# Performance work log

Hardware: AMD Instinct MI355X
Metric: run time of the kernel (lower is better)

The kernel has to match this reference:

```python
import jax, jax.numpy as jnp
import numpy as np

BS, S, DM, H = 4, 512, 512, 8
DK = DM // H
EPS = 1e-6


def setup_inputs() -> dict:
    key = jax.random.key(0)
    ks = jax.random.split(key, 11)
    sc = jnp.float32(0.02)  # small init so exp(q @ k^T) stays finite (no max-subtraction in original)
    return {
        "q": jax.random.normal(ks[0], (BS, S, DM), jnp.float32),
        "k": jax.random.normal(ks[1], (BS, S, DM), jnp.float32),
        "v": jax.random.normal(ks[2], (BS, S, DM), jnp.float32),
        "Wq": sc * jax.random.normal(ks[3], (DM, DM), jnp.float32),
        "bq": jnp.zeros((DM,), jnp.float32),
        "Wk": sc * jax.random.normal(ks[4], (DM, DM), jnp.float32),
        "bk": jnp.zeros((DM,), jnp.float32),
        "Wv": sc * jax.random.normal(ks[5], (DM, DM), jnp.float32),
        "bv": jnp.zeros((DM,), jnp.float32),
        "Wo": sc * jax.random.normal(ks[6], (DM, DM), jnp.float32),
        "bo": jnp.zeros((DM,), jnp.float32),
        "alpha": jnp.ones((DK,), jnp.float32),   # Norm.alpha over last dim (= d_k per head)
        "beta": jnp.zeros((DK,), jnp.float32),   # Norm.bias
    }


def reference(q, k, v, Wq, bq, Wk, bk, Wv, bv, Wo, bo, alpha, beta):
    # project and split heads: [bs, h, s, d_k]
    qh = (q @ Wq + bq).reshape(BS, S, H, DK).transpose(0, 2, 1, 3)
    kh = (k @ Wk + bk).reshape(BS, S, H, DK).transpose(0, 2, 1, 3)
    vh = (v @ Wv + bv).reshape(BS, S, H, DK).transpose(0, 2, 1, 3)

    # pairwise-batch exp scores: E[bq, bk, h, i, j] = exp(q[bq] @ k[bk]^T)
    E = jnp.exp(jnp.einsum('bhid,chjd->bchij', qh, kh))  # [BS, BS, H, S, S]
    # fenmu: sum over k-batch, each term scaled by sqrt(d_k) (as in original loop)
    fenmu = jnp.sqrt(jnp.float32(DK)) * E.sum(axis=1)     # [BS, H, S, S]
    # fenzi: same-batch exp scores (diagonal of pairwise tensor)
    fenzi = E[jnp.arange(BS), jnp.arange(BS)]             # [BS, H, S, S]
    R = fenzi / fenmu                                     # [BS, H, S, S]

    # per v-batch-entry score: score[bq, c] = R[bq] @ v[c]
    score = jnp.einsum('bhij,chjd->bchid', R, vh)         # [BS, BS, H, S, DK]
    sm = jax.nn.softmax(score, axis=-1)
    # Norm: torch.std is unbiased (ddof=1); eps added to std, not variance
    mu = sm.mean(axis=-1, keepdims=True)
    std = jnp.sqrt(sm.var(axis=-1, ddof=1, keepdims=True))
    ln = alpha * (sm - mu) / (std + EPS) + beta

    # output += LN(score) + q, accumulated over the v-batch loop (BS iterations)
    heads = ln.sum(axis=1) + jnp.float32(BS) * qh         # [BS, H, S, DK]
    concat = heads.transpose(0, 2, 1, 3).reshape(BS, S, DM)
    return concat @ Wo + bo
```

## Files before the change

### kernel.cpp

```cpp
#include <hip/hip_runtime.h>
#include <hip/hip_bf16.h>

#define BSZ 4
#define SEQ 512
#define DMODEL 512
#define NHEAD 8
#define DKH 64
#define EPSLN 1e-6f

typedef short bf16x8 __attribute__((ext_vector_type(8)));
typedef float f32x4 __attribute__((ext_vector_type(4)));

static __device__ __forceinline__ short f2bf(float x) {
  unsigned u = __builtin_bit_cast(unsigned, x);
  u = (u + 0x7FFFu + ((u >> 16) & 1u)) >> 16;
  return (short)u;
}
static __device__ __forceinline__ bf16x8 cvt8(float4 a, float4 b) {
  bf16x8 r;
  r[0] = f2bf(a.x); r[1] = f2bf(a.y); r[2] = f2bf(a.z); r[3] = f2bf(a.w);
  r[4] = f2bf(b.x); r[5] = f2bf(b.y); r[6] = f2bf(b.z); r[7] = f2bf(b.w);
  return r;
}
static __device__ __forceinline__ unsigned pk2(float a, float b) {
  return (unsigned)(unsigned short)f2bf(a) |
         ((unsigned)(unsigned short)f2bf(b) << 16);
}
static __device__ __forceinline__ void async_cp16(const void* g, void* l) {
  __builtin_amdgcn_global_load_lds(
      (const __attribute__((address_space(1))) unsigned int*)g,
      (__attribute__((address_space(3))) unsigned int*)l, 16, 0, 0);
}

__global__ __launch_bounds__(256) void prep_kernel(
    const float* __restrict__ q, const float* __restrict__ k,
    const float* __restrict__ v, short* __restrict__ qb,
    short* __restrict__ kb, short* __restrict__ vb,
    const float* __restrict__ Wq, const float* __restrict__ Wk,
    const float* __restrict__ Wv, const float* __restrict__ Wo,
    short* __restrict__ Wqt, short* __restrict__ Wkt,
    short* __restrict__ Wvt, short* __restrict__ Wot) {
  __shared__ float T[64][65];
  const int bx = blockIdx.x;
  if (bx < 1536) {
    const int which = bx >> 9, blk = bx & 511;
    const float* s; short* d;
    switch (which) {
      case 0: s = q; d = qb; break;
      case 1: s = k; d = kb; break;
      default: s = v; d = vb; break;
    }
    const size_t idx = (size_t)blk * 2048 + (size_t)threadIdx.x * 8;
    float4 a = *(const float4*)&s[idx];
    float4 b = *(const float4*)&s[idx + 4];
    *(bf16x8*)&d[idx] = cvt8(a, b);
    return;
  }
  const int r = bx - 1536;
  const int mat = r >> 6, m = r & 63;
  const int k0 = (m & 7) * 64, n0 = (m >> 3) * 64;
  const float* src; short* dst;
  switch (mat) {
    case 0: src = Wq; dst = Wqt; break;
    case 1: src = Wk; dst = Wkt; break;
    case 2: src = Wv; dst = Wvt; break;
    default: src = Wo; dst = Wot; break;
  }
  const int tid = threadIdx.x;
  const int n4 = (tid & 15) * 4, kk = tid >> 4;
#pragma unroll
  for (int p = 0; p < 4; ++p) {
    float4 w4 = *(const float4*)&src[(size_t)(k0 + kk + p * 16) * DMODEL + n0 + n4];
    T[kk + p * 16][n4 + 0] = w4.x;
    T[kk + p * 16][n4 + 1] = w4.y;
    T[kk + p * 16][n4 + 2] = w4.z;
    T[kk + p * 16][n4 + 3] = w4.w;
  }
  __syncthreads();
  const int k4 = (tid & 15) * 4;
#pragma unroll
  for (int p = 0; p < 4; ++p) {
    const int nn = (tid >> 4) + p * 16;
    float x0 = T[k4 + 0][nn], x1 = T[k4 + 1][nn];
    float x2 = T[k4 + 2][nn], x3 = T[k4 + 3][nn];
    uint2 u; u.x = pk2(x0, x1); u.y = pk2(x2, x3);
    *(uint2*)&dst[(size_t)(n0 + nn) * DMODEL + k0 + k4] = u;
  }
}

__device__ __forceinline__ void gemm_body(
    const short* __restrict__ A, const short* __restrict__ Wt,
    const float* __restrict__ bias, void* __restrict__ out, int omode) {
  __shared__ short As[2][128 * 32];
  __shared__ short Bs[2][128 * 32];
  const int tid = threadIdx.x;
  const int w = tid >> 6, lane = tid & 63;
  const int l15 = lane & 15, q = lane >> 4;
  const int wm = w >> 1, wn = w & 1;
  const int bn = blockIdx.x * 128, bm = blockIdx.y * 128;
  const int wu = __builtin_amdgcn_readfirstlane(w);
  const int srow = wu * 16 + (lane >> 2);
  const int sch = (lane & 3) ^ ((srow >> 1) & 3);

  f32x4 acc[4][4] = {};

#define GSTAGE(k0, buf)                                                      \
  {                                                                          \
    const short* ga0 = A + (size_t)(bm + srow) * 512 + (k0) + sch * 8;       \
    const short* ga1 = A + (size_t)(bm + srow + 64) * 512 + (k0) + sch * 8;  \
    const short* gb0 = Wt + (size_t)(bn + srow) * 512 + (k0) + sch * 8;      \
    const short* gb1 = Wt + (size_t)(bn + srow + 64) * 512 + (k0) + sch * 8; \
    async_cp16(ga0, &As[buf][wu * 512]);                                     \
    async_cp16(ga1, &As[buf][(4 + wu) * 512]);                               \
    async_cp16(gb0, &Bs[buf][wu * 512]);                                     \
    async_cp16(gb1, &Bs[buf][(4 + wu) * 512]);                               \
  }

  GSTAGE(0, 0);
  for (int ks = 0; ks < 16; ++ks) {
    __syncthreads();
    if (ks < 15) GSTAGE((ks + 1) * 32, (ks + 1) & 1);
    const short* a = As[ks & 1];
    const short* bsh = Bs[ks & 1];
    bf16x8 af[4], bfr[4];
#pragma unroll
    for (int mt = 0; mt < 4; ++mt) {
      const int ra = wm * 64 + mt * 16 + l15;
      af[mt] = *(const bf16x8*)&a[ra * 32 + (q ^ ((ra >> 1) & 3)) * 8];
    }
#pragma unroll
    for (int nt = 0; nt < 4; ++nt) {
      const int rb = wn * 64 + nt * 16 + l15;
      bfr[nt] = *(const bf16x8*)&bsh[rb * 32 + (q ^ ((rb >> 1) & 3)) * 8];
    }
#pragma unroll
    for (int mt = 0; mt < 4; ++mt)
#pragma unroll
      for (int nt = 0; nt < 4; ++nt)
        acc[mt][nt] = __builtin_amdgcn_mfma_f32_16x16x32_bf16(
            af[mt], bfr[nt], acc[mt][nt], 0, 0, 0);
  }
#undef GSTAGE

  float bv[4];
#pragma unroll
  for (int nt = 0; nt < 4; ++nt) bv[nt] = bias[bn + wn * 64 + nt * 16 + l15];
#pragma unroll
  for (int mt = 0; mt < 4; ++mt)
#pragma unroll
    for (int nt = 0; nt < 4; ++nt) {
      const int col = bn + wn * 64 + nt * 16 + l15;
#pragma unroll
      for (int r = 0; r < 4; ++r) {
        const int row = bm + wm * 64 + mt * 16 + q * 4 + r;
        const float val = acc[mt][nt][r] + bv[nt];
        if (omode == 0) {
          ((float*)out)[(size_t)row * 512 + col] = val;
        } else if (omode == 1) {
          ((short*)out)[(size_t)row * 512 + col] = f2bf(val);
        } else {
          const int cc = row >> 9, j = row & 511;
          const int hh = col >> 6, d = col & 63;
          ((short*)out)[(((size_t)(cc * 8 + hh) * 64 + d) << 9) + j] = f2bf(val);
        }
      }
    }
}

__global__ __launch_bounds__(256, 3) void proj_gemm(
    const short* qb, const short* kb, const short* vb,
    const short* Wqt, const short* Wkt, const short* Wvt,
    const float* bq, const float* bk, const float* bvs,
    float* Qp, short* Kb, short* Vt) {
  const short* A; const short* Wt; const float* bias; void* out; int omode;
  switch (blockIdx.z) {
    case 0: A = qb; Wt = Wqt; bias = bq; out = Qp; omode = 0; break;
    case 1: A = kb; Wt = Wkt; bias = bk; out = Kb; omode = 1; break;
    default: A = vb; Wt = Wvt; bias = bvs; out = Vt; omode = 2; break;
  }
  gemm_body(A, Wt, bias, out, omode);
}

__global__ __launch_bounds__(256, 3) void out_gemm(
    const short* Hc, const short* Wot, const float* bo, float* out) {
  gemm_body(Hc, Wot, bo, out, 0);
}

__global__ __launch_bounds__(256, 3) void attn2_kernel(
    const float* __restrict__ Qp, const short* __restrict__ Kb,
    const short* __restrict__ Vt, const float* __restrict__ alpha,
    const float* __restrict__ beta, short* __restrict__ Hc) {
  __shared__ __align__(16) short Stage[2][2 * 4096];
  __shared__ __align__(16) short Rs[32][72];
  __shared__ __align__(16) float xch[16 * 128];

  const int bx = blockIdx.x;
  const int h = bx & 7;
  const int b = (bx >> 3) & 3;
  const int it = bx >> 5;
  const int i0 = it * 32;
  const int tid = threadIdx.x;
  const int w = tid >> 6, lane = tid & 63;
  const int l15 = lane & 15, q = lane >> 4;
  const int wi = w >> 1, wj = w & 1;
  const int wu = __builtin_amdgcn_readfirstlane(w);

  const float* qrow =
      Qp + (size_t)(b * SEQ + i0 + wi * 16 + l15) * DMODEL + h * DKH;
  const bf16x8 aq0 = cvt8(*(const float4*)(qrow + q * 8),
                          *(const float4*)(qrow + q * 8 + 4));
  const bf16x8 aq1 = cvt8(*(const float4*)(qrow + 32 + q * 8),
                          *(const float4*)(qrow + 32 + q * 8 + 4));

  const int srow0 = wu * 8 + (lane >> 3);
  const int scol = (lane & 7) ^ (lane >> 3);

  const short* kbase_h = Kb + h * DKH;
  const short* vbase_h = Vt + (((size_t)h * DKH) << 9);

#define STG1(g0, rs, buf, tslot)                                          \
  {                                                                       \
    async_cp16((g0) + (size_t)srow0 * (rs) + scol * 8,                    \
               &Stage[buf][(tslot) * 4096 + wu * 512]);                   \
    async_cp16((g0) + (size_t)(srow0 + 32) * (rs) + scol * 8,             \
               &Stage[buf][(tslot) * 4096 + (4 + wu) * 512]);             \
  }
#define KTILE(c, j0) (kbase_h + ((size_t)((c) * SEQ) + (j0)) * DMODEL)
#define VTILE(c, j0) (vbase_h + (((size_t)((c) * NHEAD * DKH)) << 9) + (j0))

  f32x4 acc[4][4] = {};
  float sacc[2][4], ebb[2][4];

  STG1(KTILE(0, 0), DMODEL, 0, 0);
  STG1(KTILE(1, 0), DMODEL, 0, 1);

  for (int jt = 0; jt < 8; ++jt) {
    const int j0 = jt * 64;
    bf16x8 ar;
#pragma unroll
    for (int ph2 = 0; ph2 < 4; ++ph2) {
      __syncthreads();
      const int buf = ph2 & 1, nbuf = buf ^ 1;
      if (ph2 == 0) {
        STG1(KTILE(2, j0), DMODEL, nbuf, 0);
        STG1(KTILE(3, j0), DMODEL, nbuf, 1);
      } else if (ph2 == 1) {
        STG1(VTILE(0, j0), SEQ, nbuf, 0);
        STG1(VTILE(1, j0), SEQ, nbuf, 1);
      } else if (ph2 == 2) {
        STG1(VTILE(2, j0), SEQ, nbuf, 0);
        STG1(VTILE(3, j0), SEQ, nbuf, 1);
      } else if (jt < 7) {
        STG1(KTILE(0, j0 + 64), DMODEL, nbuf, 0);
        STG1(KTILE(1, j0 + 64), DMODEL, nbuf, 1);
      }
      if (ph2 < 2) {
        if (ph2 == 0) {
#pragma unroll
          for (int t = 0; t < 2; ++t)
#pragma unroll
            for (int r = 0; r < 4; ++r) { sacc[t][r] = 0.0f; ebb[t][r] = 0.0f; }
        }
#pragma unroll
        for (int ct = 0; ct < 2; ++ct) {
          const int c = ph2 * 2 + ct;
          const short* S = &Stage[buf][ct * 4096];
#pragma unroll
          for (int ntl = 0; ntl < 2; ++ntl) {
            const int row = (wj * 2 + ntl) * 16 + l15;
            const int p0 = q ^ (l15 & 7);
            bf16x8 b0 = *(const bf16x8*)&S[row * 64 + p0 * 8];
            bf16x8 b1 = *(const bf16x8*)&S[row * 64 + (p0 ^ 4) * 8];
            f32x4 s = {};
            s = __builtin_amdgcn_mfma_f32_16x16x32_bf16(aq0, b0, s, 0, 0, 0);
            s = __builtin_amdgcn_mfma_f32_16x16x32_bf16(aq1, b1, s, 0, 0, 0);
#pragma unroll
            for (int r = 0; r < 4; ++r) {
              const float e = __expf(s[r]);
              sacc[ntl][r] += e;
              ebb[ntl][r] = (c == b) ? e : ebb[ntl][r];
            }
          }
        }
        if (ph2 == 1) {
#pragma unroll
          for (int ntl = 0; ntl < 2; ++ntl)
#pragma unroll
            for (int r = 0; r < 4; ++r)
              Rs[wi * 16 + q * 4 + r][(wj * 2 + ntl) * 16 + l15] =
                  f2bf(ebb[ntl][r] / (8.0f * sacc[ntl][r]));
        }
      } else {
        if (ph2 == 2) ar = *(const bf16x8*)&Rs[wi * 16 + l15][wj * 32 + q * 8];
#pragma unroll
        for (int ct = 0; ct < 2; ++ct) {
          const int c = (ph2 - 2) * 2 + ct;
          const short* S = &Stage[buf][ct * 4096];
#pragma unroll
          for (int nt = 0; nt < 4; ++nt) {
            const int row = nt * 16 + l15;
            const int pb = (wj * 4 + q) ^ (l15 & 7);
            bf16x8 bv = *(const bf16x8*)&S[row * 64 + pb * 8];
            acc[c][nt] = __builtin_amdgcn_mfma_f32_16x16x32_bf16(
                ar, bv, acc[c][nt], 0, 0, 0);
          }
        }
      }
    }
  }
#undef STG1
#undef KTILE
#undef VTILE

#pragma unroll
  for (int c = 0; c < BSZ; ++c) {
    if (wj == 1) {
#pragma unroll
      for (int nt = 0; nt < 4; ++nt)
#pragma unroll
        for (int r = 0; r < 4; ++r)
          xch[(nt * 4 + r) * 128 + wi * 64 + lane] = acc[c][nt][r];
    }
    __syncthreads();
    if (wj == 0) {
#pragma unroll
      for (int nt = 0; nt < 4; ++nt)
#pragma unroll
        for (int r = 0; r < 4; ++r)
          acc[c][nt][r] += xch[(nt * 4 + r) * 128 + wi * 64 + lane];
    }
    __syncthreads();
  }

  if (wj == 0) {
    float al[4], be[4];
#pragma unroll
    for (int nt = 0; nt < 4; ++nt) {
      al[nt] = alpha[nt * 16 + l15];
      be[nt] = beta[nt * 16 + l15];
    }
    float hacc[4][4] = {};
#pragma unroll
    for (int c = 0; c < BSZ; ++c) {
#pragma unroll
      for (int r = 0; r < 4; ++r) {
        float e0 = __expf(acc[c][0][r]), e1 = __expf(acc[c][1][r]);
        float e2 = __expf(acc[c][2][r]), e3 = __expf(acc[c][3][r]);
        float es = e0 + e1 + e2 + e3;
#pragma unroll
        for (int m = 8; m >= 1; m >>= 1) es += __shfl_xor(es, m);
        const float inv = 1.0f / es;
        const float d0 = e0 * inv - 0.015625f, d1 = e1 * inv - 0.015625f;
        const float d2 = e2 * inv - 0.015625f, d3 = e3 * inv - 0.015625f;
        float sq = d0 * d0 + d1 * d1 + d2 * d2 + d3 * d3;
#pragma unroll
        for (int m = 8; m >= 1; m >>= 1) sq += __shfl_xor(sq, m);
        const float rs = 1.0f / (sqrtf(sq * (1.0f / 63.0f)) + EPSLN);
        hacc[r][0] += al[0] * d0 * rs + be[0];
        hacc[r][1] += al[1] * d1 * rs + be[1];
        hacc[r][2] += al[2] * d2 * rs + be[2];
        hacc[r][3] += al[3] * d3 * rs + be[3];
      }
    }
#pragma unroll
    for (int r = 0; r < 4; ++r) {
      const size_t rowoff =
          (size_t)(b * SEQ + i0 + wi * 16 + q * 4 + r) * DMODEL + h * DKH;
#pragma unroll
      for (int nt = 0; nt < 4; ++nt) {
        const int d = nt * 16 + l15;
        const float o = hacc[r][nt] + 4.0f * Qp[rowoff + d];
        Hc[rowoff + d] = f2bf(o);
      }
    }
  }
}

extern "C" void kernel_launch(void* const* d_in, const int* in_sizes, int n_in,
                              void* d_out, int out_size, void* d_ws,
                              size_t ws_size, hipStream_t stream) {
  (void)in_sizes; (void)n_in; (void)out_size; (void)ws_size;
  const float* q = (const float*)d_in[0];
  const float* k = (const float*)d_in[1];
  const float* v = (const float*)d_in[2];
  const float* Wq = (const float*)d_in[3];
  const float* bq = (const float*)d_in[4];
  const float* Wk = (const float*)d_in[5];
  const float* bk = (const float*)d_in[6];
  const float* Wv = (const float*)d_in[7];
  const float* bv = (const float*)d_in[8];
  const float* Wo = (const float*)d_in[9];
  const float* bo = (const float*)d_in[10];
  const float* alpha = (const float*)d_in[11];
  const float* beta = (const float*)d_in[12];
  float* out = (float*)d_out;

  char* wsb = (char*)d_ws;
  short* qb = (short*)(wsb);
  short* kb = (short*)(wsb + (2u << 20));
  short* vb = (short*)(wsb + (4u << 20));
  float* Qp = (float*)(wsb + (6u << 20));
  short* Kb = (short*)(wsb + (10u << 20));
  short* Vtg = (short*)(wsb + (12u << 20));
  short* Hc = (short*)(wsb + (14u << 20));
  short* Wqt = (short*)(wsb + (16u << 20));
  short* Wkt = (short*)(wsb + (16u << 20) + (512u << 10));
  short* Wvt = (short*)(wsb + (17u << 20));
  short* Wot = (short*)(wsb + (17u << 20) + (512u << 10));

  prep_kernel<<<dim3(1792), 256, 0, stream>>>(q, k, v, qb, kb, vb,
                                              Wq, Wk, Wv, Wo,
                                              Wqt, Wkt, Wvt, Wot);
  proj_gemm<<<dim3(4, 16, 3), 256, 0, stream>>>(qb, kb, vb, Wqt, Wkt, Wvt,
                                                bq, bk, bv, Qp, Kb, Vtg);
  attn2_kernel<<<dim3(512), 256, 0, stream>>>(Qp, Kb, Vtg, alpha, beta, Hc);
  out_gemm<<<dim3(4, 16), 256, 0, stream>>>(Hc, Wot, bo, out);
}
```

Baseline: 147.1 us.

## Split attention key range across warps with per-warp async ring buffers

Restructures the attention kernel so each of the four warps owns a 32-column slice of the key range for all 32 query rows. Each warp streams its own K/V tiles through a private double-buffered LDS ring, using vmcnt waits in place of block-wide barriers in the main loop. Partial P·V accumulators are then reduced across warps through LDS in a rotated pattern, and each warp computes softmax/LayerNorm for one v-batch. The output is written with vectorized bf16 stores. This trades more registers (launch bounds drop to 2 blocks per SM) and an extra LDS reduction for removing per-phase __syncthreads and reusing each K/V fragment across two query tiles.

```diff
diff --git a/kernel.cpp b/kernel.cpp
--- a/kernel.cpp
+++ b/kernel.cpp
@@ -186,13 +186,12 @@
   gemm_body(Hc, Wot, bo, out, 0);
 }
 
-__global__ __launch_bounds__(256, 3) void attn2_kernel(
+__global__ __launch_bounds__(256, 2) void attn4_kernel(
     const float* __restrict__ Qp, const short* __restrict__ Kb,
     const short* __restrict__ Vt, const float* __restrict__ alpha,
     const float* __restrict__ beta, short* __restrict__ Hc) {
-  __shared__ __align__(16) short Stage[2][2 * 4096];
-  __shared__ __align__(16) short Rs[32][72];
-  __shared__ __align__(16) float xch[16 * 128];
+  __shared__ __align__(16) short Ring[4][2][2048];
+  __shared__ __align__(16) short Rsw[4][32 * 40];
 
   const int bx = blockIdx.x;
   const int h = bx & 7;
@@ -202,150 +201,211 @@
   const int tid = threadIdx.x;
   const int w = tid >> 6, lane = tid & 63;
   const int l15 = lane & 15, q = lane >> 4;
-  const int wi = w >> 1, wj = w & 1;
   const int wu = __builtin_amdgcn_readfirstlane(w);
-
-  const float* qrow =
-      Qp + (size_t)(b * SEQ + i0 + wi * 16 + l15) * DMODEL + h * DKH;
-  const bf16x8 aq0 = cvt8(*(const float4*)(qrow + q * 8),
-                          *(const float4*)(qrow + q * 8 + 4));
-  const bf16x8 aq1 = cvt8(*(const float4*)(qrow + 32 + q * 8),
-                          *(const float4*)(qrow + 32 + q * 8 + 4));
-
-  const int srow0 = wu * 8 + (lane >> 3);
+  short* ring0 = &Ring[wu][0][0];
+  short* ring1 = &Ring[wu][1][0];
+  short* rsw = &Rsw[wu][0];
+
+  bf16x8 aq[2][2];
+#pragma unroll
+  for (int mi = 0; mi < 2; ++mi) {
+    const float* qrow =
+        Qp + (size_t)(b * SEQ + i0 + mi * 16 + l15) * DMODEL + h * DKH;
+    aq[mi][0] = cvt8(*(const float4*)(qrow + q * 8),
+                     *(const float4*)(qrow + q * 8 + 4));
+    aq[mi][1] = cvt8(*(const float4*)(qrow + 32 + q * 8),
+                     *(const float4*)(qrow + 32 + q * 8 + 4));
+  }
+
   const int scol = (lane & 7) ^ (lane >> 3);
-
-  const short* kbase_h = Kb + h * DKH;
-  const short* vbase_h = Vt + (((size_t)h * DKH) << 9);
-
-#define STG1(g0, rs, buf, tslot)                                          \
-  {                                                                       \
-    async_cp16((g0) + (size_t)srow0 * (rs) + scol * 8,                    \
-               &Stage[buf][(tslot) * 4096 + wu * 512]);                   \
-    async_cp16((g0) + (size_t)(srow0 + 32) * (rs) + scol * 8,             \
-               &Stage[buf][(tslot) * 4096 + (4 + wu) * 512]);             \
-  }
-#define KTILE(c, j0) (kbase_h + ((size_t)((c) * SEQ) + (j0)) * DMODEL)
-#define VTILE(c, j0) (vbase_h + (((size_t)((c) * NHEAD * DKH)) << 9) + (j0))
-
-  f32x4 acc[4][4] = {};
-  float sacc[2][4], ebb[2][4];
-
-  STG1(KTILE(0, 0), DMODEL, 0, 0);
-  STG1(KTILE(1, 0), DMODEL, 0, 1);
-
-  for (int jt = 0; jt < 8; ++jt) {
-    const int j0 = jt * 64;
-    bf16x8 ar;
-#pragma unroll
-    for (int ph2 = 0; ph2 < 4; ++ph2) {
-      __syncthreads();
-      const int buf = ph2 & 1, nbuf = buf ^ 1;
-      if (ph2 == 0) {
-        STG1(KTILE(2, j0), DMODEL, nbuf, 0);
-        STG1(KTILE(3, j0), DMODEL, nbuf, 1);
-      } else if (ph2 == 1) {
-        STG1(VTILE(0, j0), SEQ, nbuf, 0);
-        STG1(VTILE(1, j0), SEQ, nbuf, 1);
-      } else if (ph2 == 2) {
-        STG1(VTILE(2, j0), SEQ, nbuf, 0);
-        STG1(VTILE(3, j0), SEQ, nbuf, 1);
-      } else if (jt < 7) {
-        STG1(KTILE(0, j0 + 64), DMODEL, nbuf, 0);
-        STG1(KTILE(1, j0 + 64), DMODEL, nbuf, 1);
+  int koff[4], voff[4];
+#pragma unroll
+  for (int s = 0; s < 4; ++s) {
+    koff[s] = ((s >> 1) * 64 + w * 16 + (s & 1) * 8 + (lane >> 3)) * 512 +
+              h * 64 + scol * 8;
+    const int Lc = (lane & 3) ^ ((lane >> 3) & 3);
+    voff[s] = h * 32768 + (s * 16 + (lane >> 2)) * 512 + w * 16 +
+              (Lc >> 1) * 64 + (Lc & 1) * 8;
+  }
+
+#define STAGEK(t, c, sp)                                             \
+  do {                                                               \
+    const short* gK = Kb + (c) * 262144 + (t) * 65536;               \
+    async_cp16(gK + koff[0], (sp));                                  \
+    async_cp16(gK + koff[1], (sp) + 512);                            \
+    async_cp16(gK + koff[2], (sp) + 1024);                           \
+    async_cp16(gK + koff[3], (sp) + 1536);                           \
+  } while (0)
+#define STAGEV(t, c, sp)                                             \
+  do {                                                               \
+    const short* gV = Vt + (c) * 262144 + (t) * 128;                 \
+    async_cp16(gV + voff[0], (sp));                                  \
+    async_cp16(gV + voff[1], (sp) + 512);                            \
+    async_cp16(gV + voff[2], (sp) + 1024);                           \
+    async_cp16(gV + voff[3], (sp) + 1536);                           \
+  } while (0)
+
+  f32x4 acc[4][2][4] = {};
+  STAGEK(0, 0, ring0);
+
+  for (int t = 0; t < 4; ++t) {
+    float sacc[2][2][4], ebb[2][2][4];
+    bf16x8 ar[2];
+#pragma unroll
+    for (int ph = 0; ph < 8; ++ph) {
+      short* cur = (ph & 1) ? ring1 : ring0;
+      short* nxt = (ph & 1) ? ring0 : ring1;
+      if (ph < 3) {
+        STAGEK(t, ph + 1, nxt);
+      } else if (ph == 3) {
+        STAGEV(t, 0, nxt);
+      } else if (ph < 7) {
+        STAGEV(t, ph - 3, nxt);
+      } else if (t < 3) {
+        STAGEK(t + 1, 0, nxt);
       }
-      if (ph2 < 2) {
-        if (ph2 == 0) {
-#pragma unroll
-          for (int t = 0; t < 2; ++t)
-#pragma unroll
-            for (int r = 0; r < 4; ++r) { sacc[t][r] = 0.0f; ebb[t][r] = 0.0f; }
-        }
-#pragma unroll
-        for (int ct = 0; ct < 2; ++ct) {
-          const int c = ph2 * 2 + ct;
-          const short* S = &Stage[buf][ct * 4096];
-#pragma unroll
-          for (int ntl = 0; ntl < 2; ++ntl) {
-            const int row = (wj * 2 + ntl) * 16 + l15;
-            const int p0 = q ^ (l15 & 7);
-            bf16x8 b0 = *(const bf16x8*)&S[row * 64 + p0 * 8];
-            bf16x8 b1 = *(const bf16x8*)&S[row * 64 + (p0 ^ 4) * 8];
-            f32x4 s = {};
-            s = __builtin_amdgcn_mfma_f32_16x16x32_bf16(aq0, b0, s, 0, 0, 0);
-            s = __builtin_amdgcn_mfma_f32_16x16x32_bf16(aq1, b1, s, 0, 0, 0);
-#pragma unroll
-            for (int r = 0; r < 4; ++r) {
-              const float e = __expf(s[r]);
-              sacc[ntl][r] += e;
-              ebb[ntl][r] = (c == b) ? e : ebb[ntl][r];
-            }
+      if (ph == 7 && t == 3) {
+        asm volatile("s_waitcnt vmcnt(0)" ::: "memory");
+      } else {
+        asm volatile("s_waitcnt vmcnt(4)" ::: "memory");
+      }
+      if (ph < 4) {
+        const int c = ph;
+        if (ph == 0) {
+#pragma unroll
+          for (int s2 = 0; s2 < 2; ++s2)
+#pragma unroll
+            for (int mi = 0; mi < 2; ++mi)
+#pragma unroll
+              for (int r = 0; r < 4; ++r) {
+                sacc[s2][mi][r] = 0.0f;
+                ebb[s2][mi][r] = 0.0f;
+              }
+        }
+#pragma unroll
+        for (int sub = 0; sub < 2; ++sub) {
+          const int row = sub * 16 + l15;
+          const int p0 = q ^ (l15 & 7);
+          bf16x8 b0 = *(const bf16x8*)&cur[row * 64 + p0 * 8];
+          bf16x8 b1 = *(const bf16x8*)&cur[row * 64 + (p0 ^ 4) * 8];
+          f32x4 s0 = {}, s1 = {};
+          s0 = __builtin_amdgcn_mfma_f32_16x16x32_bf16(aq[0][0], b0, s0, 0, 0, 0);
+          s0 = __builtin_amdgcn_mfma_f32_16x16x32_bf16(aq[0][1], b1, s0, 0, 0, 0);
+          s1 = __builtin_amdgcn_mfma_f32_16x16x32_bf16(aq[1][0], b0, s1, 0, 0, 0);
+          s1 = __builtin_amdgcn_mfma_f32_16x16x32_bf16(aq[1][1], b1, s1, 0, 0, 0);
+#pragma unroll
+          for (int r = 0; r < 4; ++r) {
+            const float e0 = __expf(s0[r]);
+            const float e1 = __expf(s1[r]);
+            sacc[sub][0][r] += e0;
+            sacc[sub][1][r] += e1;
+            ebb[sub][0][r] = (c == b) ? e0 : ebb[sub][0][r];
+            ebb[sub][1][r] = (c == b) ? e1 : ebb[sub][1][r];
           }
         }
-        if (ph2 == 1) {
-#pragma unroll
-          for (int ntl = 0; ntl < 2; ++ntl)
-#pragma unroll
-            for (int r = 0; r < 4; ++r)
-              Rs[wi * 16 + q * 4 + r][(wj * 2 + ntl) * 16 + l15] =
-                  f2bf(ebb[ntl][r] / (8.0f * sacc[ntl][r]));
+        if (ph == 3) {
+#pragma unroll
+          for (int sub = 0; sub < 2; ++sub)
+#pragma unroll
+            for (int mi = 0; mi < 2; ++mi)
+#pragma unroll
+              for (int r = 0; r < 4; ++r)
+                rsw[(mi * 16 + q * 4 + r) * 40 + sub * 16 + l15] =
+                    f2bf(ebb[sub][mi][r] / (8.0f * sacc[sub][mi][r]));
         }
       } else {
-        if (ph2 == 2) ar = *(const bf16x8*)&Rs[wi * 16 + l15][wj * 32 + q * 8];
-#pragma unroll
-        for (int ct = 0; ct < 2; ++ct) {
-          const int c = (ph2 - 2) * 2 + ct;
-          const short* S = &Stage[buf][ct * 4096];
-#pragma unroll
-          for (int nt = 0; nt < 4; ++nt) {
-            const int row = nt * 16 + l15;
-            const int pb = (wj * 4 + q) ^ (l15 & 7);
-            bf16x8 bv = *(const bf16x8*)&S[row * 64 + pb * 8];
-            acc[c][nt] = __builtin_amdgcn_mfma_f32_16x16x32_bf16(
-                ar, bv, acc[c][nt], 0, 0, 0);
-          }
+        const int c = ph - 4;
+        if (ph == 4) {
+          ar[0] = *(const bf16x8*)&rsw[(0 * 16 + l15) * 40 + q * 8];
+          ar[1] = *(const bf16x8*)&rsw[(1 * 16 + l15) * 40 + q * 8];
+        }
+#pragma unroll
+        for (int nt = 0; nt < 4; ++nt) {
+          const int d = nt * 16 + l15;
+          const int pv = q ^ ((l15 >> 1) & 3);
+          bf16x8 bvv = *(const bf16x8*)&cur[d * 32 + pv * 8];
+          acc[c][0][nt] = __builtin_amdgcn_mfma_f32_16x16x32_bf16(
+              ar[0], bvv, acc[c][0][nt], 0, 0, 0);
+          acc[c][1][nt] = __builtin_amdgcn_mfma_f32_16x16x32_bf16(
+              ar[1], bvv, acc[c][1][nt], 0, 0, 0);
         }
       }
     }
   }
-#undef STG1
-#undef KTILE
-#undef VTILE
-
-#pragma unroll
-  for (int c = 0; c < BSZ; ++c) {
-    if (wj == 1) {
-#pragma unroll
-      for (int nt = 0; nt < 4; ++nt)
-#pragma unroll
-        for (int r = 0; r < 4; ++r)
-          xch[(nt * 4 + r) * 128 + wi * 64 + lane] = acc[c][nt][r];
-    }
+#undef STAGEK
+#undef STAGEV
+
+  float* xch = (float*)&Ring[0][0][0];
+#define XWR(A, reg)                                                        \
+  do {                                                                     \
+    _Pragma("unroll") for (int mi = 0; mi < 2; ++mi)                       \
+        _Pragma("unroll") for (int nt = 0; nt < 4; ++nt)                   \
+        *(f32x4*)&xch[(reg) * 2048 + (mi * 4 + nt) * 256 + lane * 4] =     \
+            A[mi][nt];                                                     \
+  } while (0)
+#define XADD(A, reg)                                                       \
+  do {                                                                     \
+    _Pragma("unroll") for (int mi = 0; mi < 2; ++mi)                       \
+        _Pragma("unroll") for (int nt = 0; nt < 4; ++nt) {                 \
+      f32x4 o =                                                            \
+          *(f32x4*)&xch[(reg) * 2048 + (mi * 4 + nt) * 256 + lane * 4];    \
+      A[mi][nt] += o;                                                      \
+    }                                                                      \
+  } while (0)
+
+  __syncthreads();
+#pragma unroll
+  for (int k = 1; k < 4; ++k) {
+    if (w == 0) XWR(acc[(0 + k) & 3], (0 + k) & 3);
+    else if (w == 1) XWR(acc[(1 + k) & 3], (1 + k) & 3);
+    else if (w == 2) XWR(acc[(2 + k) & 3], (2 + k) & 3);
+    else XWR(acc[(3 + k) & 3], (3 + k) & 3);
     __syncthreads();
-    if (wj == 0) {
-#pragma unroll
-      for (int nt = 0; nt < 4; ++nt)
-#pragma unroll
-        for (int r = 0; r < 4; ++r)
-          acc[c][nt][r] += xch[(nt * 4 + r) * 128 + wi * 64 + lane];
-    }
+    if (w == 0) XADD(acc[0], 0);
+    else if (w == 1) XADD(acc[1], 1);
+    else if (w == 2) XADD(acc[2], 2);
+    else XADD(acc[3], 3);
     __syncthreads();
   }
-
-  if (wj == 0) {
+#undef XWR
+#undef XADD
+
+  f32x4 sc[2][4];
+  if (w == 0) {
+#pragma unroll
+    for (int mi = 0; mi < 2; ++mi)
+#pragma unroll
+      for (int nt = 0; nt < 4; ++nt) sc[mi][nt] = acc[0][mi][nt];
+  } else if (w == 1) {
+#pragma unroll
+    for (int mi = 0; mi < 2; ++mi)
+#pragma unroll
+      for (int nt = 0; nt < 4; ++nt) sc[mi][nt] = acc[1][mi][nt];
+  } else if (w == 2) {
+#pragma unroll
+    for (int mi = 0; mi < 2; ++mi)
+#pragma unroll
+      for (int nt = 0; nt < 4; ++nt) sc[mi][nt] = acc[2][mi][nt];
+  } else {
+#pragma unroll
+    for (int mi = 0; mi < 2; ++mi)
+#pragma unroll
+      for (int nt = 0; nt < 4; ++nt) sc[mi][nt] = acc[3][mi][nt];
+  }
+
+  {
     float al[4], be[4];
 #pragma unroll
     for (int nt = 0; nt < 4; ++nt) {
       al[nt] = alpha[nt * 16 + l15];
       be[nt] = beta[nt * 16 + l15];
     }
-    float hacc[4][4] = {};
-#pragma unroll
-    for (int c = 0; c < BSZ; ++c) {
+#pragma unroll
+    for (int mi = 0; mi < 2; ++mi)
 #pragma unroll
       for (int r = 0; r < 4; ++r) {
-        float e0 = __expf(acc[c][0][r]), e1 = __expf(acc[c][1][r]);
-        float e2 = __expf(acc[c][2][r]), e3 = __expf(acc[c][3][r]);
+        float e0 = __expf(sc[mi][0][r]), e1 = __expf(sc[mi][1][r]);
+        float e2 = __expf(sc[mi][2][r]), e3 = __expf(sc[mi][3][r]);
         float es = e0 + e1 + e2 + e3;
 #pragma unroll
         for (int m = 8; m >= 1; m >>= 1) es += __shfl_xor(es, m);
@@ -356,23 +416,33 @@
 #pragma unroll
         for (int m = 8; m >= 1; m >>= 1) sq += __shfl_xor(sq, m);
         const float rs = 1.0f / (sqrtf(sq * (1.0f / 63.0f)) + EPSLN);
-        hacc[r][0] += al[0] * d0 * rs + be[0];
-        hacc[r][1] += al[1] * d1 * rs + be[1];
-        hacc[r][2] += al[2] * d2 * rs + be[2];
-        hacc[r][3] += al[3] * d3 * rs + be[3];
+        const int i = mi * 16 + q * 4 + r;
+        float* o = &xch[w * 2048 + i * 64 + l15];
+        o[0] = al[0] * d0 * rs + be[0];
+        o[16] = al[1] * d1 * rs + be[1];
+        o[32] = al[2] * d2 * rs + be[2];
+        o[48] = al[3] * d3 * rs + be[3];
       }
-    }
-#pragma unroll
-    for (int r = 0; r < 4; ++r) {
-      const size_t rowoff =
-          (size_t)(b * SEQ + i0 + wi * 16 + q * 4 + r) * DMODEL + h * DKH;
-#pragma unroll
-      for (int nt = 0; nt < 4; ++nt) {
-        const int d = nt * 16 + l15;
-        const float o = hacc[r][nt] + 4.0f * Qp[rowoff + d];
-        Hc[rowoff + d] = f2bf(o);
-      }
-    }
+  }
+  __syncthreads();
+
+  {
+    const int i2 = tid >> 3, d8 = (tid & 7) * 8;
+    f32x4 sA = {}, sB = {};
+#pragma unroll
+    for (int reg = 0; reg < 4; ++reg) {
+      sA += *(f32x4*)&xch[reg * 2048 + i2 * 64 + d8];
+      sB += *(f32x4*)&xch[reg * 2048 + i2 * 64 + d8 + 4];
+    }
+    const size_t rowoff = (size_t)(b * SEQ + i0 + i2) * DMODEL + h * DKH + d8;
+    float4 q0 = *(const float4*)&Qp[rowoff];
+    float4 q1 = *(const float4*)&Qp[rowoff + 4];
+    float4 a, bb;
+    a.x = sA[0] + 4.0f * q0.x; a.y = sA[1] + 4.0f * q0.y;
+    a.z = sA[2] + 4.0f * q0.z; a.w = sA[3] + 4.0f * q0.w;
+    bb.x = sB[0] + 4.0f * q1.x; bb.y = sB[1] + 4.0f * q1.y;
+    bb.z = sB[2] + 4.0f * q1.z; bb.w = sB[3] + 4.0f * q1.w;
+    *(bf16x8*)&Hc[rowoff] = cvt8(a, bb);
   }
 }
 
@@ -413,6 +483,6 @@
                                               Wqt, Wkt, Wvt, Wot);
   proj_gemm<<<dim3(4, 16, 3), 256, 0, stream>>>(qb, kb, vb, Wqt, Wkt, Wvt,
                                                 bq, bk, bv, Qp, Kb, Vtg);
-  attn2_kernel<<<dim3(512), 256, 0, stream>>>(Qp, Kb, Vtg, alpha, beta, Hc);
+  attn4_kernel<<<dim3(512), 256, 0, stream>>>(Qp, Kb, Vtg, alpha, beta, Hc);
   out_gemm<<<dim3(4, 16), 256, 0, stream>>>(Hc, Wot, bo, out);
 }
```

New measurement: 142.4 us, median of 2. -3.2%, faster.
